# Performance work log

Measured on AMD Instinct MI355X. Metric: run time of the kernel, lower is better.

## Reference

```python
import jax, jax.numpy as jnp
import numpy as np

L, E, H, S, V, F = 8, 1024, 16, 2048, 32000, 4096
NEG = -1e9  # mask value used by the original (triu * -1e9)


def setup_inputs() -> dict:
    key = jax.random.key(0)
    ks = jax.random.split(key, 10)
    s = 0.02  # init scale to keep activations stable without residuals/LN
    return {
        "inpt": jax.random.randint(ks[0], (S,), 0, V, dtype=jnp.int32),
        "num_heads": H,
        "emb_table": jax.random.normal(ks[1], (V, E), dtype=jnp.float32) * s,
        "Wq": jax.random.normal(ks[2], (L, E, E), dtype=jnp.float32) * s,
        "bq": jnp.zeros((L, E), dtype=jnp.float32),
        "Wk": jax.random.normal(ks[3], (L, E, E), dtype=jnp.float32) * s,
        "bk": jnp.zeros((L, E), dtype=jnp.float32),
        "Wv": jax.random.normal(ks[4], (L, E, E), dtype=jnp.float32) * s,
        "bv": jnp.zeros((L, E), dtype=jnp.float32),
        "W1": jax.random.normal(ks[5], (L, E, F), dtype=jnp.float32) * s,
        "b1": jnp.zeros((L, F), dtype=jnp.float32),
        "W2": jax.random.normal(ks[6], (L, F, E), dtype=jnp.float32) * s,
        "b2": jnp.zeros((L, E), dtype=jnp.float32),
        "Wout": jax.random.normal(ks[7], (E, V), dtype=jnp.float32) * s,
    }


def reference(inpt, num_heads, emb_table, Wq, bq, Wk, bk, Wv, bv, W1, b1, W2, b2, Wout):
    x = emb_table[inpt]                      # [S, E] embedding lookup
    seq_len, emb_dim = x.shape
    head_dim = emb_dim // num_heads
    scale = head_dim ** 0.5
    n_layers = Wq.shape[0]
    # additive causal mask, exactly as torch.triu(ones)*-1e9
    mask = jnp.triu(jnp.full((seq_len, seq_len), NEG, dtype=x.dtype), k=1)

    for l in range(n_layers):  # fixed small layer count
        q = (x @ Wq[l] + bq[l]).reshape(seq_len, num_heads, head_dim).transpose(1, 0, 2)
        k = (x @ Wk[l] + bk[l]).reshape(seq_len, num_heads, head_dim).transpose(1, 0, 2)
        v = (x @ Wv[l] + bv[l]).reshape(seq_len, num_heads, head_dim).transpose(1, 0, 2)
        scores = jnp.einsum('hqd,hkd->hqk', q, k) / scale + mask  # [H, S, S]
        probs = jax.nn.softmax(scores, axis=-1)
        attn = jnp.einsum('hqk,hkd->hqd', probs, v)               # [H, S, D]
        attn = attn.transpose(1, 0, 2).reshape(seq_len, emb_dim)  # [S, E]
        # NOTE: original has no residual connection; x is replaced by FFN(attn)
        x = jax.nn.relu(attn @ W1[l] + b1[l]) @ W2[l] + b2[l]

    return x @ Wout  # [S, V] logits (no bias, no softmax in original forward)
```

## Files before the change

kernel.cpp:

```cpp
#include <hip/hip_runtime.h>
#include <hip/hip_fp16.h>


#define SS 2048
#define EE 1024
#define NH 16
#define FF 4096
#define NV 32000
#define NL 8

typedef _Float16 f16;
typedef _Float16 f16x8 __attribute__((ext_vector_type(8)));
typedef _Float16 f16x4 __attribute__((ext_vector_type(4)));
typedef float f32x4 __attribute__((ext_vector_type(4)));

#define CS 4096.0f
#define INV_CS 0.000244140625f
#define SCORE_SCALE 7.450580596923828e-09f

__device__ __forceinline__ void gload16(const void* g, void* lds) {
    __builtin_amdgcn_global_load_lds(
        (const __attribute__((address_space(1))) unsigned int*)g,
        (__attribute__((address_space(3))) unsigned int*)lds, 16, 0, 0);
}

#define BAR do { asm volatile("" ::: "memory"); __builtin_amdgcn_s_barrier(); } while (0)

__global__ void k_embed(const int* __restrict__ ids, const float* __restrict__ emb,
                        f16* __restrict__ xh) {
    int s = blockIdx.x;
    int e = threadIdx.x * 4;
    const float4 v = *(const float4*)&emb[(size_t)ids[s] * EE + e];
    f16x4 h;
    h[0] = (f16)(v.x * CS); h[1] = (f16)(v.y * CS);
    h[2] = (f16)(v.z * CS); h[3] = (f16)(v.w * CS);
    *(f16x4*)&xh[(size_t)s * EE + e] = h;
}

__device__ __forceinline__ void tr64(const float* __restrict__ in, f16* __restrict__ out,
                                     int ldi, int ldo, int bx, int by) {
    __shared__ float tl[64][65];
    const int tx = threadIdx.x & 15, ty = threadIdx.x >> 4;
#pragma unroll
    for (int i = 0; i < 4; i++) {
        float4 v = *(const float4*)&in[(size_t)(by + ty * 4 + i) * ldi + bx + tx * 4];
        tl[ty * 4 + i][tx * 4 + 0] = v.x;
        tl[ty * 4 + i][tx * 4 + 1] = v.y;
        tl[ty * 4 + i][tx * 4 + 2] = v.z;
        tl[ty * 4 + i][tx * 4 + 3] = v.w;
    }
    __syncthreads();
#pragma unroll
    for (int i = 0; i < 4; i++) {
        f16x4 h;
#pragma unroll
        for (int j = 0; j < 4; j++) h[j] = (f16)tl[tx * 4 + j][ty * 4 + i];
        *(f16x4*)&out[(size_t)(bx + ty * 4 + i) * ldo + by + tx * 4] = h;
    }
}

__global__ void k_trW(const float* __restrict__ Wq, const float* __restrict__ Wk,
                      const float* __restrict__ Wv, const float* __restrict__ W1,
                      const float* __restrict__ W2,
                      const float* __restrict__ bq, const float* __restrict__ bk,
                      const float* __restrict__ bv,
                      f16* __restrict__ wqkvt, f16* __restrict__ w1t,
                      f16* __restrict__ w2t, float* __restrict__ bqkv) {
    int b = blockIdx.x;
    if (b == 2816) {
        int i = threadIdx.x;
#pragma unroll
        for (int j = 0; j < 12; j++) {
            int idx = j * 256 + i;
            bqkv[idx] = idx < EE ? bq[idx] : (idx < 2 * EE ? bk[idx - EE] : bv[idx - 2 * EE]);
        }
        return;
    }
    if (b < 768) {
        int s = b >> 8, t2 = b & 255;
        tr64(s == 0 ? Wq : (s == 1 ? Wk : Wv), wqkvt + (size_t)s * EE * EE,
             EE, EE, (t2 & 15) * 64, (t2 >> 4) * 64);
    } else if (b < 1792) {
        int t2 = b - 768;
        tr64(W1, w1t, FF, EE, (t2 & 63) * 64, (t2 >> 6) * 64);
    } else {
        int t2 = b - 1792;
        tr64(W2, w2t, EE, FF, (t2 & 15) * 64, (t2 >> 4) * 64);
    }
}

__global__ void k_trOut(const float* __restrict__ in, f16* __restrict__ out) {
    int b = blockIdx.x;
    tr64(in, out, NV, EE, (b % 500) * 64, (b / 500) * 64);
}

__global__ void k_combine4(const float* __restrict__ part, const float* __restrict__ bias,
                           f16* __restrict__ out) {
    const size_t sz = (size_t)SS * EE;
    int i = (blockIdx.x * 256 + threadIdx.x) * 4;
    float4 a = *(const float4*)&part[i];
    float4 b = *(const float4*)&part[i + sz];
    float4 c = *(const float4*)&part[i + 2 * sz];
    float4 d = *(const float4*)&part[i + 3 * sz];
    float4 bb = *(const float4*)&bias[i & (EE - 1)];
    f16x4 h;
    h[0] = (f16)(a.x + b.x + c.x + d.x + bb.x * CS);
    h[1] = (f16)(a.y + b.y + c.y + d.y + bb.y * CS);
    h[2] = (f16)(a.z + b.z + c.z + d.z + bb.z * CS);
    h[3] = (f16)(a.w + b.w + c.w + d.w + bb.w * CS);
    *(f16x4*)&out[i] = h;
}

template<int BM, int BN, int TAG>
__global__ __launch_bounds__((BM == 128) ? 256 : 512, 2) void k_gemm(
    const f16* __restrict__ A, const f16* __restrict__ B,
    const float* __restrict__ bias, f16* __restrict__ Ch, float* __restrict__ Cf,
    f16* __restrict__ VtOut,
    int M, int N, int Kstride, int Ksub, int nm, int nn, int kch,
    float bscale, float oscale, int relu) {
    constexpr int WR = (BM == 256) ? ((BN == 256) ? 2 : 4) : 2;
    constexpr int WC = (BN == 256) ? 4 : 2;
    constexpr int NW = WR * WC;
    constexpr int THREADS = NW * 64;
    constexpr int MR = BM / WR / 16;
    constexpr int RPC = THREADS / 8;
    constexpr int ACALLS = BM / RPC;
    constexpr int BCALLS = BN / RPC;
    constexpr int LPT = ACALLS + BCALLS;

    __shared__ f16 As[2][BM * 64];
    __shared__ f16 Bs[2][BN * 64];

    const int t = threadIdx.x;
    const int l = t & 63, w = t >> 6;
    const int lr = l & 15, lc = l >> 4;

    const int nwg = nm * nn * kch;
    const int q8 = nwg >> 3, r8 = nwg & 7;
    const int xcd = blockIdx.x & 7, lid = blockIdx.x >> 3;
    const int wgid = (xcd < r8 ? xcd * (q8 + 1) : r8 * (q8 + 1) + (xcd - r8) * q8) + lid;
    const int kc = wgid / (nm * nn);
    const int rem = wgid - kc * (nm * nn);
    const int m0 = (rem % nm) * BM, n0 = (rem / nm) * BN;

    const f16* Ab = A + (size_t)kc * Ksub;
    const f16* Bb = B + (size_t)kc * Ksub;
    float* Cfb = Cf ? Cf + (size_t)kc * M * N : nullptr;

    const int wr = w / WC, wc = w % WC;

    f32x4 acc[MR][4] = {};

    const int srow = t >> 3;
    const int scol = 8 * ((t & 7) ^ (srow & 7));
    const int NT = Ksub / 64;

#define STAGE(bb, tt_) { \
    const size_t kof = (size_t)(tt_) * 64 + scol; \
    _Pragma("unroll") \
    for (int c = 0; c < ACALLS; c++) \
        gload16(Ab + (size_t)(m0 + c * RPC + srow) * Kstride + kof, \
                (char*)As[bb] + c * (RPC * 128) + w * 1024); \
    _Pragma("unroll") \
    for (int c = 0; c < BCALLS; c++) \
        gload16(Bb + (size_t)(n0 + c * RPC + srow) * Kstride + kof, \
                (char*)Bs[bb] + c * (RPC * 128) + w * 1024); }

    STAGE(0, 0)
    STAGE(1, 1)
    asm volatile("s_waitcnt vmcnt(%0)" :: "n"(LPT) : "memory");
    BAR;

    int cur = 0;
    for (int tt = 0; tt < NT; ++tt) {
        const f16* pA = As[cur];
        const f16* pB = Bs[cur];
#pragma unroll
        for (int ks = 0; ks < 2; ks++) {
            f16x8 af[MR], bf[4];
#pragma unroll
            for (int m = 0; m < MR; m++) {
                const int row = wr * (MR * 16) + m * 16 + lr;
                af[m] = *(const f16x8*)&pA[row * 64 + 8 * ((ks * 4 + lc) ^ (row & 7))];
            }
#pragma unroll
            for (int n = 0; n < 4; n++) {
                const int row = wc * 64 + n * 16 + lr;
                bf[n] = *(const f16x8*)&pB[row * 64 + 8 * ((ks * 4 + lc) ^ (row & 7))];
            }
            __builtin_amdgcn_s_setprio(1);
#pragma unroll
            for (int m = 0; m < MR; m++)
#pragma unroll
                for (int n = 0; n < 4; n++)
                    acc[m][n] = __builtin_amdgcn_mfma_f32_16x16x32_f16(af[m], bf[n], acc[m][n], 0, 0, 0);
            __builtin_amdgcn_s_setprio(0);
        }
        BAR;
        if (tt + 2 < NT) {
            STAGE(cur, tt + 2)
            asm volatile("s_waitcnt vmcnt(%0)" :: "n"(LPT) : "memory");
        } else if (tt + 1 < NT) {
            asm volatile("s_waitcnt vmcnt(0)" ::: "memory");
        }
        BAR;
        cur ^= 1;
    }
#undef STAGE

#pragma unroll
    for (int m = 0; m < MR; m++)
#pragma unroll
        for (int n = 0; n < 4; n++) {
            const int row0 = m0 + wr * (MR * 16) + m * 16 + lc * 4;
            const int col = n0 + wc * 64 + n * 16 + lr;
            float v[4];
#pragma unroll
            for (int r = 0; r < 4; r++) {
                v[r] = acc[m][n][r];
                if (bias) v[r] += bias[col] * bscale;
                if (relu) v[r] = fmaxf(v[r], 0.0f);
            }
            if (VtOut && col >= 2 * EE) {
                f16x4 h4;
#pragma unroll
                for (int r = 0; r < 4; r++) h4[r] = (f16)v[r];
                *(f16x4*)&VtOut[(size_t)(col - 2 * EE) * SS + row0] = h4;
            } else if (Ch) {
#pragma unroll
                for (int r = 0; r < 4; r++)
                    Ch[(size_t)(row0 + r) * N + col] = (f16)v[r];
            } else {
#pragma unroll
                for (int r = 0; r < 4; r++)
                    Cfb[(size_t)(row0 + r) * N + col] = v[r] * oscale;
            }
        }
}

__global__ __launch_bounds__(512, 2) void k_gemm4p(
    const f16* __restrict__ A, const f16* __restrict__ B, float* __restrict__ Cf,
    int N, int K, int nm, int nn, float oscale) {
    __shared__ f16 As[2][256 * 64];
    __shared__ f16 Bs[2][256 * 64];
    const int t = threadIdx.x;
    const int l = t & 63, w = t >> 6;
    const int lr = l & 15, lc = l >> 4;

    const int nwg = nm * nn;
    const int q8 = nwg >> 3, r8 = nwg & 7;
    const int xcd = blockIdx.x & 7, lid = blockIdx.x >> 3;
    const int wgid = (xcd < r8 ? xcd * (q8 + 1) : r8 * (q8 + 1) + (xcd - r8) * q8) + lid;
    const int m0 = (wgid % nm) * 256, n0 = (wgid / nm) * 256;

    const int wr = w >> 2, wc = w & 3;

    f32x4 acc[8][4] = {};
    f16x8 aF[2][4], bF[2][4];

    const int srow = t >> 3;
    const int scol = 8 * ((t & 7) ^ (srow & 7));
    const int NT = K / 64;

#define SG_A(bb, tt_, c) \
    gload16(A + (size_t)(m0 + (c) * 64 + srow) * K + (size_t)(tt_) * 64 + scol, \
            (char*)As[bb] + (c) * 8192 + w * 1024);
#define SG_B(bb, tt_, c) \
    gload16(B + (size_t)(n0 + (c) * 64 + srow) * K + (size_t)(tt_) * 64 + scol, \
            (char*)Bs[bb] + (c) * 8192 + w * 1024);

#define LDA_HALF(pA_, mh) { _Pragma("unroll") \
    for (int ks = 0; ks < 2; ks++) _Pragma("unroll") \
    for (int m = 0; m < 4; m++) { \
        const int row = wr * 128 + ((mh) * 4 + m) * 16 + lr; \
        aF[ks][m] = *(const f16x8*)&pA_[row * 64 + 8 * ((ks * 4 + lc) ^ (row & 7))]; } }

#define LDB_PAIR(pB_, nb) { _Pragma("unroll") \
    for (int ks = 0; ks < 2; ks++) _Pragma("unroll") \
    for (int j = 0; j < 2; j++) { \
        const int row = wc * 64 + ((nb) + j) * 16 + lr; \
        bF[ks][(nb) + j] = *(const f16x8*)&pB_[row * 64 + 8 * ((ks * 4 + lc) ^ (row & 7))]; } }

#define PH_MMA(mb, nb) { __builtin_amdgcn_s_setprio(1); \
    _Pragma("unroll") for (int ks = 0; ks < 2; ks++) \
    _Pragma("unroll") for (int m = 0; m < 4; m++) \
    _Pragma("unroll") for (int j = 0; j < 2; j++) \
        acc[(mb) + m][(nb) + j] = __builtin_amdgcn_mfma_f32_16x16x32_f16( \
            aF[ks][m], bF[ks][(nb) + j], acc[(mb) + m][(nb) + j], 0, 0, 0); \
    __builtin_amdgcn_s_setprio(0); }

#pragma unroll
    for (int c = 0; c < 4; c++) { SG_A(0, 0, c) SG_B(0, 0, c) }
#pragma unroll
    for (int c = 0; c < 4; c++) { SG_A(1, 1, c) SG_B(1, 1, c) }
    asm volatile("s_waitcnt vmcnt(8)" ::: "memory");
    BAR;

    int cur = 0;
    for (int tt = 0; tt < NT; ++tt) {
        const f16* pA = As[cur];
        const f16* pB = Bs[cur];
        const bool pre = (tt + 2 < NT);

        LDA_HALF(pA, 0)
        LDB_PAIR(pB, 0)
        BAR;
        PH_MMA(0, 0)
        BAR;

        LDB_PAIR(pB, 2)
        if (pre) { SG_A(cur, tt + 2, 0) SG_A(cur, tt + 2, 2) }
        BAR;
        PH_MMA(0, 2)
        BAR;

        LDA_HALF(pA, 1)
        if (pre) { SG_B(cur, tt + 2, 0) SG_B(cur, tt + 2, 1)
                   SG_B(cur, tt + 2, 2) SG_B(cur, tt + 2, 3) }
        BAR;
        PH_MMA(4, 0)
        BAR;

        if (pre) {
            SG_A(cur, tt + 2, 1) SG_A(cur, tt + 2, 3)
            asm volatile("s_waitcnt vmcnt(8)" ::: "memory");
        } else if (tt + 1 < NT) {
            asm volatile("s_waitcnt vmcnt(0)" ::: "memory");
        }
        BAR;
        PH_MMA(4, 2)
        BAR;

        cur ^= 1;
    }
#undef SG_A
#undef SG_B
#undef LDA_HALF
#undef LDB_PAIR
#undef PH_MMA

#pragma unroll
    for (int m = 0; m < 8; m++)
#pragma unroll
        for (int n = 0; n < 4; n++) {
            const int row0 = m0 + wr * 128 + m * 16 + lc * 4;
            const int col = n0 + wc * 64 + n * 16 + lr;
#pragma unroll
            for (int r = 0; r < 4; r++)
                Cf[(size_t)(row0 + r) * N + col] = acc[m][n][r] * oscale;
        }
}

__global__ __launch_bounds__(256) void k_flash(
    const f16* __restrict__ qkv, const f16* __restrict__ vt, f16* __restrict__ attn) {
    __shared__ f16 Ks[2][4096];
    __shared__ f16 Vs[2][4096];
    __shared__ f16 Ps[4096];
    const int h = blockIdx.x;
    const int qb = (SS / 64 - 1) - blockIdx.y;
    const int t = threadIdx.x, l = t & 63, w = t >> 6;
    const int lr = l & 15, lc = l >> 4;
    const int q0 = qb * 64;
    const int qrow = q0 + w * 16 + lr;

    f16x8 qf0 = *(const f16x8*)&qkv[(size_t)qrow * 3072 + h * 64 + lc * 8];
    f16x8 qf1 = *(const f16x8*)&qkv[(size_t)qrow * 3072 + h * 64 + 32 + lc * 8];

    f32x4 o[4] = {};
    float mrun[4], lrun[4];
#pragma unroll
    for (int r = 0; r < 4; r++) { mrun[r] = -__builtin_inff(); lrun[r] = 0.0f; }

    const int krow = t >> 3;
    const int kscol = 8 * ((t & 7) ^ (krow & 7));
    const f16* gK = qkv + EE + h * 64;
    const f16* gV = vt + (size_t)(h * 64) * SS;
    f16* Pw = &Ps[w * 16 * 64];
    const int psw = (lr & 7) << 4;

#define FSTAGE(bb, kt_) { \
    char* dK = (char*)Ks[bb] + w * 1024; \
    char* dV = (char*)Vs[bb] + w * 1024; \
    gload16(gK + (size_t)((kt_) * 64 + krow) * 3072 + kscol, dK); \
    gload16(gK + (size_t)((kt_) * 64 + krow + 32) * 3072 + kscol, dK + 4096); \
    gload16(gV + (size_t)krow * SS + (kt_) * 64 + kscol, dV); \
    gload16(gV + (size_t)(krow + 32) * SS + (kt_) * 64 + kscol, dV + 4096); }

    const int nkt = qb + 1;
    FSTAGE(0, 0)
    FSTAGE(1, 1)
    asm volatile("s_waitcnt vmcnt(4)" ::: "memory");
    __builtin_amdgcn_s_barrier();

    int cur = 0;
    for (int kt = 0; kt < nkt; kt++) {
        f32x4 sc[4];
        __builtin_amdgcn_s_setprio(1);
#pragma unroll
        for (int kj = 0; kj < 4; kj++) {
            const int krw = kj * 16 + lr;
            const int sw = krw & 7;
            f16x8 kb0 = *(const f16x8*)&Ks[cur][krw * 64 + 8 * (lc ^ sw)];
            f16x8 kb1 = *(const f16x8*)&Ks[cur][krw * 64 + 8 * ((lc + 4) ^ sw)];
            f32x4 z = {};
            z = __builtin_amdgcn_mfma_f32_16x16x32_f16(qf0, kb0, z, 0, 0, 0);
            z = __builtin_amdgcn_mfma_f32_16x16x32_f16(qf1, kb1, z, 0, 0, 0);
            sc[kj] = z;
        }
        __builtin_amdgcn_s_setprio(0);

        const bool diag = (kt == qb);
#pragma unroll
        for (int kj = 0; kj < 4; kj++)
#pragma unroll
            for (int r = 0; r < 4; r++) {
                float v = sc[kj][r] * SCORE_SCALE;
                if (diag) {
                    int qq = w * 16 + lc * 4 + r;
                    int kk = kj * 16 + lr;
                    if (kk > qq) v = -__builtin_inff();
                }
                sc[kj][r] = v;
            }

#pragma unroll
        for (int r = 0; r < 4; r++) {
            float mt = fmaxf(fmaxf(sc[0][r], sc[1][r]), fmaxf(sc[2][r], sc[3][r]));
            mt = fmaxf(mt, __shfl_xor(mt, 1));
            mt = fmaxf(mt, __shfl_xor(mt, 2));
            mt = fmaxf(mt, __shfl_xor(mt, 4));
            mt = fmaxf(mt, __shfl_xor(mt, 8));
            float mnew = fmaxf(mrun[r], mt);
            float alpha = __expf(mrun[r] - mnew);
            float psum = 0.0f;
#pragma unroll
            for (int kj = 0; kj < 4; kj++) {
                float p = __expf(sc[kj][r] - mnew);
                sc[kj][r] = p;
                psum += p;
            }
            psum += __shfl_xor(psum, 1);
            psum += __shfl_xor(psum, 2);
            psum += __shfl_xor(psum, 4);
            psum += __shfl_xor(psum, 8);
            lrun[r] = lrun[r] * alpha + psum;
            mrun[r] = mnew;
#pragma unroll
            for (int dj = 0; dj < 4; dj++) o[dj][r] *= alpha;
        }

#pragma unroll
        for (int kj = 0; kj < 4; kj++)
#pragma unroll
            for (int r = 0; r < 4; r++) {
                int prow = lc * 4 + r;
                int pb = prow * 128 + ((kj * 16 + lr) * 2 ^ ((prow & 7) << 4));
                *(f16*)((char*)Pw + pb) = (f16)sc[kj][r];
            }

        __builtin_amdgcn_s_setprio(1);
#pragma unroll
        for (int s2 = 0; s2 < 2; s2++) {
            f16x8 pa = *(const f16x8*)((const char*)Pw + lr * 128 + (((lc + 4 * s2) * 16) ^ psw));
#pragma unroll
            for (int dj = 0; dj < 4; dj++) {
                const int vrow = dj * 16 + lr;
                f16x8 vb = *(const f16x8*)&Vs[cur][vrow * 64 + 8 * ((lc + 4 * s2) ^ (vrow & 7))];
                o[dj] = __builtin_amdgcn_mfma_f32_16x16x32_f16(pa, vb, o[dj], 0, 0, 0);
            }
        }
        __builtin_amdgcn_s_setprio(0);

        asm volatile("" ::: "memory");
        __builtin_amdgcn_s_barrier();
        if (kt + 2 < nkt) {
            FSTAGE(cur, kt + 2)
            asm volatile("s_waitcnt vmcnt(4)" ::: "memory");
        } else if (kt + 1 < nkt) {
            asm volatile("s_waitcnt vmcnt(0)" ::: "memory");
        }
        __builtin_amdgcn_s_barrier();
        cur ^= 1;
    }
#undef FSTAGE

#pragma unroll
    for (int dj = 0; dj < 4; dj++)
#pragma unroll
        for (int r = 0; r < 4; r++) {
            float v = o[dj][r] / lrun[r];
            attn[(size_t)(q0 + w * 16 + lc * 4 + r) * EE + h * 64 + dj * 16 + lr] = (f16)v;
        }
}

extern "C" void kernel_launch(void* const* d_in, const int* in_sizes, int n_in,
                              void* d_out, int out_size, void* d_ws, size_t ws_size,
                              hipStream_t stream) {
    const int*   ids  = (const int*)d_in[0];
    const float* emb  = (const float*)d_in[2];
    const float* Wq   = (const float*)d_in[3];
    const float* bq   = (const float*)d_in[4];
    const float* Wk   = (const float*)d_in[5];
    const float* bk   = (const float*)d_in[6];
    const float* Wv   = (const float*)d_in[7];
    const float* bv   = (const float*)d_in[8];
    const float* W1   = (const float*)d_in[9];
    const float* b1   = (const float*)d_in[10];
    const float* W2   = (const float*)d_in[11];
    const float* b2   = (const float*)d_in[12];
    const float* Wout = (const float*)d_in[13];
    float* out = (float*)d_out;

    char* p = (char*)d_ws;
    f16* xh    = (f16*)p; p += (size_t)SS * EE * 2;
    f16* qkvh  = (f16*)p; p += (size_t)SS * 3 * EE * 2;
    f16* vt    = (f16*)p; p += (size_t)EE * SS * 2;
    f16* attn  = (f16*)p; p += (size_t)SS * EE * 2;
    f16* h1    = (f16*)p; p += (size_t)SS * FF * 2;
    f16* wqkvt = (f16*)p; p += (size_t)3 * EE * EE * 2;
    f16* w1t   = (f16*)p; p += (size_t)FF * EE * 2;
    f16* w2t   = (f16*)p; p += (size_t)EE * FF * 2;
    f16* woutt = (f16*)p; p += (size_t)NV * EE * 2;
    float* part = (float*)p; p += (size_t)4 * SS * EE * 4;
    float* bqkv = (float*)p; p += 3 * EE * 4;

    k_embed<<<SS, 256, 0, stream>>>(ids, emb, xh);

    for (int l = 0; l < NL; l++) {
        k_trW<<<2817, 256, 0, stream>>>(
            Wq + (size_t)l * EE * EE, Wk + (size_t)l * EE * EE, Wv + (size_t)l * EE * EE,
            W1 + (size_t)l * EE * FF, W2 + (size_t)l * FF * EE,
            bq + l * EE, bk + l * EE, bv + l * EE,
            wqkvt, w1t, w2t, bqkv);

        k_gemm<256, 128, 1><<<8 * 24, 512, 0, stream>>>(
            xh, wqkvt, bqkv, qkvh, nullptr, vt, SS, 3 * EE, EE, EE, 8, 24, 1, CS, 1.0f, 0);

        k_flash<<<dim3(NH, SS / 64), 256, 0, stream>>>(qkvh, vt, attn);

        k_gemm<256, 128, 2><<<8 * 32, 512, 0, stream>>>(
            attn, w1t, b1 + (size_t)l * FF, h1, nullptr, nullptr, SS, FF, EE, EE, 8, 32, 1, CS, 1.0f, 1);

        k_gemm<256, 128, 3><<<8 * 8 * 4, 512, 0, stream>>>(
            h1, w2t, nullptr, nullptr, part, nullptr, SS, EE, FF, FF / 4, 8, 8, 4, 0.0f, 1.0f, 0);
        k_combine4<<<SS * EE / 1024, 256, 0, stream>>>(part, b2 + (size_t)l * EE, xh);
    }

    k_trOut<<<8000, 256, 0, stream>>>(Wout, woutt);
    k_gemm4p<<<8 * 125, 512, 0, stream>>>(xh, woutt, out, NV, EE, 8, 125, INV_CS);
}
```

Baseline: 1.523 ms.

## Widen flash-attention KV tiles to 128 with lazy rescale and exp2 softmax

The flash attention kernel now processes 128 keys per iteration instead of 64, halving loop iterations, barriers and online-softmax bookkeeping per query block. The score scale folds in log2(e) so the kernel can use exp2f. Rescaling of the running max and accumulator is skipped unless some row's new max exceeds the old one by a threshold (FA4-style lazy rescale). Query blocks are interleaved across blockIdx.y to balance causal work. The changes raise LDS use and register pressure, and diagonal tiles now waste more masked work.

```diff
diff --git a/kernel.cpp b/kernel.cpp
--- a/kernel.cpp
+++ b/kernel.cpp
@@ -17,6 +17,7 @@
 #define CS 4096.0f
 #define INV_CS 0.000244140625f
 #define SCORE_SCALE 7.450580596923828e-09f
+#define SCORE_SCALE2 1.0748631e-08f
 
 __device__ __forceinline__ void gload16(const void* g, void* lds) {
     __builtin_amdgcn_global_load_lds(
@@ -353,11 +354,12 @@
 
 __global__ __launch_bounds__(256) void k_flash(
     const f16* __restrict__ qkv, const f16* __restrict__ vt, f16* __restrict__ attn) {
-    __shared__ f16 Ks[2][4096];
-    __shared__ f16 Vs[2][4096];
-    __shared__ f16 Ps[4096];
+    __shared__ f16 Ks[2][128 * 64];
+    __shared__ f16 Vs[2][64 * 128];
+    __shared__ f16 Ps[4 * 16 * 128];
     const int h = blockIdx.x;
-    const int qb = (SS / 64 - 1) - blockIdx.y;
+    const int y = blockIdx.y;
+    const int qb = (y < 16) ? (31 - 2 * y) : (2 * (y - 16));
     const int t = threadIdx.x, l = t & 63, w = t >> 6;
     const int lr = l & 15, lc = l >> 4;
     const int q0 = qb * 64;
@@ -373,31 +375,33 @@
 
     const int krow = t >> 3;
     const int kscol = 8 * ((t & 7) ^ (krow & 7));
+    const int vrow = t >> 4;
+    const int vscol = 8 * ((t & 15) ^ (vrow & 7));
     const f16* gK = qkv + EE + h * 64;
     const f16* gV = vt + (size_t)(h * 64) * SS;
-    f16* Pw = &Ps[w * 16 * 64];
+    f16* Pw = &Ps[w * 16 * 128];
     const int psw = (lr & 7) << 4;
 
 #define FSTAGE(bb, kt_) { \
-    char* dK = (char*)Ks[bb] + w * 1024; \
-    char* dV = (char*)Vs[bb] + w * 1024; \
-    gload16(gK + (size_t)((kt_) * 64 + krow) * 3072 + kscol, dK); \
-    gload16(gK + (size_t)((kt_) * 64 + krow + 32) * 3072 + kscol, dK + 4096); \
-    gload16(gV + (size_t)krow * SS + (kt_) * 64 + kscol, dV); \
-    gload16(gV + (size_t)(krow + 32) * SS + (kt_) * 64 + kscol, dV + 4096); }
-
-    const int nkt = qb + 1;
+    _Pragma("unroll") \
+    for (int c = 0; c < 4; c++) { \
+        gload16(gK + (size_t)((kt_) * 128 + c * 32 + krow) * 3072 + kscol, \
+                (char*)Ks[bb] + c * 4096 + w * 1024); \
+        gload16(gV + (size_t)(c * 16 + vrow) * SS + (kt_) * 128 + vscol, \
+                (char*)Vs[bb] + c * 4096 + w * 1024); } }
+
+    const int nkt = (qb >> 1) + 1;
     FSTAGE(0, 0)
     FSTAGE(1, 1)
-    asm volatile("s_waitcnt vmcnt(4)" ::: "memory");
+    asm volatile("s_waitcnt vmcnt(8)" ::: "memory");
     __builtin_amdgcn_s_barrier();
 
     int cur = 0;
     for (int kt = 0; kt < nkt; kt++) {
-        f32x4 sc[4];
+        f32x4 sc[8];
         __builtin_amdgcn_s_setprio(1);
 #pragma unroll
-        for (int kj = 0; kj < 4; kj++) {
+        for (int kj = 0; kj < 8; kj++) {
             const int krw = kj * 16 + lr;
             const int sw = krw & 7;
             f16x8 kb0 = *(const f16x8*)&Ks[cur][krw * 64 + 8 * (lc ^ sw)];
@@ -409,33 +413,50 @@
         }
         __builtin_amdgcn_s_setprio(0);
 
-        const bool diag = (kt == qb);
-#pragma unroll
-        for (int kj = 0; kj < 4; kj++)
+        const bool diag = (kt == nkt - 1);
+#pragma unroll
+        for (int kj = 0; kj < 8; kj++)
 #pragma unroll
             for (int r = 0; r < 4; r++) {
-                float v = sc[kj][r] * SCORE_SCALE;
+                float v = sc[kj][r] * SCORE_SCALE2;
                 if (diag) {
-                    int qq = w * 16 + lc * 4 + r;
-                    int kk = kj * 16 + lr;
+                    int kk = kt * 128 + kj * 16 + lr;
+                    int qq = q0 + w * 16 + lc * 4 + r;
                     if (kk > qq) v = -__builtin_inff();
                 }
                 sc[kj][r] = v;
             }
 
+        float mt[4];
 #pragma unroll
         for (int r = 0; r < 4; r++) {
-            float mt = fmaxf(fmaxf(sc[0][r], sc[1][r]), fmaxf(sc[2][r], sc[3][r]));
-            mt = fmaxf(mt, __shfl_xor(mt, 1));
-            mt = fmaxf(mt, __shfl_xor(mt, 2));
-            mt = fmaxf(mt, __shfl_xor(mt, 4));
-            mt = fmaxf(mt, __shfl_xor(mt, 8));
-            float mnew = fmaxf(mrun[r], mt);
-            float alpha = __expf(mrun[r] - mnew);
+            float m2 = fmaxf(fmaxf(fmaxf(sc[0][r], sc[1][r]), fmaxf(sc[2][r], sc[3][r])),
+                             fmaxf(fmaxf(sc[4][r], sc[5][r]), fmaxf(sc[6][r], sc[7][r])));
+            m2 = fmaxf(m2, __shfl_xor(m2, 1));
+            m2 = fmaxf(m2, __shfl_xor(m2, 2));
+            m2 = fmaxf(m2, __shfl_xor(m2, 4));
+            m2 = fmaxf(m2, __shfl_xor(m2, 8));
+            mt[r] = m2;
+        }
+        bool need = (mt[0] > mrun[0] + 11.0f) || (mt[1] > mrun[1] + 11.0f) ||
+                    (mt[2] > mrun[2] + 11.0f) || (mt[3] > mrun[3] + 11.0f);
+        if (__any(need)) {
+#pragma unroll
+            for (int r = 0; r < 4; r++) {
+                float mnew = fmaxf(mrun[r], mt[r]);
+                float alpha = exp2f(mrun[r] - mnew);
+                lrun[r] *= alpha;
+                mrun[r] = mnew;
+#pragma unroll
+                for (int dj = 0; dj < 4; dj++) o[dj][r] *= alpha;
+            }
+        }
+#pragma unroll
+        for (int r = 0; r < 4; r++) {
             float psum = 0.0f;
 #pragma unroll
-            for (int kj = 0; kj < 4; kj++) {
-                float p = __expf(sc[kj][r] - mnew);
+            for (int kj = 0; kj < 8; kj++) {
+                float p = exp2f(sc[kj][r] - mrun[r]);
                 sc[kj][r] = p;
                 psum += p;
             }
@@ -443,29 +464,26 @@
             psum += __shfl_xor(psum, 2);
             psum += __shfl_xor(psum, 4);
             psum += __shfl_xor(psum, 8);
-            lrun[r] = lrun[r] * alpha + psum;
-            mrun[r] = mnew;
-#pragma unroll
-            for (int dj = 0; dj < 4; dj++) o[dj][r] *= alpha;
-        }
-
-#pragma unroll
-        for (int kj = 0; kj < 4; kj++)
+            lrun[r] += psum;
+        }
+
+#pragma unroll
+        for (int kj = 0; kj < 8; kj++)
 #pragma unroll
             for (int r = 0; r < 4; r++) {
                 int prow = lc * 4 + r;
-                int pb = prow * 128 + ((kj * 16 + lr) * 2 ^ ((prow & 7) << 4));
+                int pb = prow * 256 + (((kj * 16 + lr) * 2) ^ ((prow & 7) << 4));
                 *(f16*)((char*)Pw + pb) = (f16)sc[kj][r];
             }
 
         __builtin_amdgcn_s_setprio(1);
 #pragma unroll
-        for (int s2 = 0; s2 < 2; s2++) {
-            f16x8 pa = *(const f16x8*)((const char*)Pw + lr * 128 + (((lc + 4 * s2) * 16) ^ psw));
+        for (int s2 = 0; s2 < 4; s2++) {
+            f16x8 pa = *(const f16x8*)((const char*)Pw + lr * 256 + (((lc + 4 * s2) * 16) ^ psw));
 #pragma unroll
             for (int dj = 0; dj < 4; dj++) {
-                const int vrow = dj * 16 + lr;
-                f16x8 vb = *(const f16x8*)&Vs[cur][vrow * 64 + 8 * ((lc + 4 * s2) ^ (vrow & 7))];
+                const int vr = dj * 16 + lr;
+                f16x8 vb = *(const f16x8*)&Vs[cur][vr * 128 + 8 * ((s2 * 4 + lc) ^ (vr & 7))];
                 o[dj] = __builtin_amdgcn_mfma_f32_16x16x32_f16(pa, vb, o[dj], 0, 0, 0);
             }
         }
@@ -475,7 +493,7 @@
         __builtin_amdgcn_s_barrier();
         if (kt + 2 < nkt) {
             FSTAGE(cur, kt + 2)
-            asm volatile("s_waitcnt vmcnt(4)" ::: "memory");
+            asm volatile("s_waitcnt vmcnt(8)" ::: "memory");
         } else if (kt + 1 < nkt) {
             asm volatile("s_waitcnt vmcnt(0)" ::: "memory");
         }
```

Result: faster. 1.440 ms (-5.4%).
